# Performance work log

Hardware: AMD Instinct MI355X
Metric: run time of the kernel (lower is better)

The kernel has to match this reference:

```python
import jax, jax.numpy as jnp
import numpy as np
import math

HID = 256      # hidden_dim
POS = 32       # pos_dim (hardcoded num_pos_feats=32 in pos2embed call)
HEADS = 4
DH = HID // HEADS
B = 8          # number of ragged batches
N = 2048       # points per batch (inputs and queries, equal counts)
LN_EPS = 1e-5


def pos2embed(pos, num_pos_feats=POS):
    # pos: [..., 3] -> [..., 3*num_pos_feats]; faithfully keeps the original
    # bug where pos_z's cos half uses pos_x.
    pos = pos * (2.0 * math.pi)
    dim_t = jnp.arange(num_pos_feats, dtype=jnp.float32)
    dim_t = 2.0 * jnp.floor(dim_t / 2.0) / num_pos_feats + 1.0
    px = pos[..., 0, None] / dim_t
    py = pos[..., 1, None] / dim_t
    pz = pos[..., 2, None] / dim_t
    def interleave(s, c):
        return jnp.stack((s, c), axis=-1).reshape(*s.shape[:-1], -1)
    ex = interleave(jnp.sin(px[..., 0::2]), jnp.cos(px[..., 1::2]))
    ey = interleave(jnp.sin(py[..., 0::2]), jnp.cos(py[..., 1::2]))
    ez = interleave(jnp.sin(pz[..., 0::2]), jnp.cos(px[..., 1::2]))  # original bug
    return jnp.concatenate((ey, ex, ez), axis=-1)


def setup_inputs() -> dict:
    key = jax.random.key(0)
    ks = jax.random.split(key, 16)
    inputs = jax.random.normal(ks[0], (B * N, HID), jnp.float32)
    Q_in = jax.random.normal(ks[1], (B * N, HID), jnp.float32)
    bid = jnp.repeat(jnp.arange(B, dtype=jnp.float32), N)[:, None]
    input_coords = jnp.concatenate([bid, jax.random.uniform(ks[2], (B * N, 3), jnp.float32)], -1)
    Q_in_coords = jnp.concatenate([bid, jax.random.uniform(ks[3], (B * N, 3), jnp.float32)], -1)
    s = 0.02
    Wq = jax.random.normal(ks[4], (HID, HID + POS), jnp.float32) * s
    Wk = jax.random.normal(ks[5], (HID, HID + POS), jnp.float32) * s
    Wv = jax.random.normal(ks[6], (HID, HID + POS), jnp.float32) * s
    in_proj_w = jax.random.normal(ks[7], (3 * HID, HID), jnp.float32) * s
    in_proj_b = jnp.zeros((3 * HID,), jnp.float32)
    out_proj_w = jax.random.normal(ks[8], (HID, HID), jnp.float32) * s
    out_proj_b = jnp.zeros((HID,), jnp.float32)
    ln_g = jnp.ones((HID,), jnp.float32)
    ln_b = jnp.zeros((HID,), jnp.float32)
    pe_w1 = jax.random.normal(ks[9], (POS, POS * 3), jnp.float32) * s
    pe_b1 = jnp.zeros((POS,), jnp.float32)
    pe_w2 = jax.random.normal(ks[10], (POS, POS), jnp.float32) * s
    pe_b2 = jnp.zeros((POS,), jnp.float32)
    return dict(inputs=inputs, Q_in=Q_in, input_coords=input_coords, Q_in_coords=Q_in_coords,
                Wq=Wq, Wk=Wk, Wv=Wv, in_proj_w=in_proj_w, in_proj_b=in_proj_b,
                out_proj_w=out_proj_w, out_proj_b=out_proj_b, ln_g=ln_g, ln_b=ln_b,
                pe_w1=pe_w1, pe_b1=pe_b1, pe_w2=pe_w2, pe_b2=pe_b2)


def reference(inputs, Q_in, input_coords, Q_in_coords, Wq, Wk, Wv,
              in_proj_w, in_proj_b, out_proj_w, out_proj_b, ln_g, ln_b,
              pe_w1, pe_b1, pe_w2, pe_b2):
    # Equal per-batch counts let the ragged per-batch loop be one batched op.
    def pos_mlp(coords):  # [BN,4] -> [B,N,POS]
        e = pos2embed(coords[:, 1:], POS)                   # [BN, 3*POS]
        h = jax.nn.relu(e @ pe_w1.T + pe_b1)
        return (h @ pe_w2.T + pe_b2).reshape(B, N, POS)

    xb = inputs.reshape(B, N, HID)
    qb = Q_in.reshape(B, N, HID)
    ip = jnp.concatenate([xb, pos_mlp(input_coords)], -1)   # [B,N,HID+POS]
    qp = jnp.concatenate([qb, pos_mlp(Q_in_coords)], -1)

    Q = jnp.einsum('bnc,hc->bnh', qp, Wq)
    K = jnp.einsum('bnc,hc->bnh', ip, Wk)
    V = jnp.einsum('bnc,hc->bnh', ip, Wv)

    # nn.MultiheadAttention: its own in_proj on top of Q/K/V, then out_proj
    wq, wk, wv = in_proj_w[:HID], in_proj_w[HID:2 * HID], in_proj_w[2 * HID:]
    bq, bk, bv = in_proj_b[:HID], in_proj_b[HID:2 * HID], in_proj_b[2 * HID:]
    q = (Q @ wq.T + bq).reshape(B, N, HEADS, DH)
    k = (K @ wk.T + bk).reshape(B, N, HEADS, DH)
    v = (V @ wv.T + bv).reshape(B, N, HEADS, DH)

    scores = jnp.einsum('bqhd,bkhd->bhqk', q, k) / math.sqrt(DH)
    attn = jax.nn.softmax(scores, axis=-1)
    o = jnp.einsum('bhqk,bkhd->bqhd', attn, v).reshape(B, N, HID)
    o = o @ out_proj_w.T + out_proj_b

    # residual + LayerNorm (dropout is identity in eval)
    y = qb + o
    mu = y.mean(-1, keepdims=True)
    var = ((y - mu) ** 2).mean(-1, keepdims=True)
    yn = (y - mu) / jnp.sqrt(var + LN_EPS) * ln_g + ln_b
    return yn.reshape(B * N, HID)
```

## Files before the change

### kernel.cpp

```cpp
#include <hip/hip_runtime.h>
#include <math.h>

#define HID 256
#define CIN 288
#define NTOK 16384
#define NSEQ 2048
#define NH 4
#define DHD 64
#define TWO_PI 6.2831853071795864769f

typedef __attribute__((ext_vector_type(8))) short bf16x8;
typedef __attribute__((ext_vector_type(4))) float f32x4;
typedef __attribute__((ext_vector_type(4))) unsigned short u16x4;

__device__ __forceinline__ ushort f2bf(float x) {
    unsigned u = __float_as_uint(x);
    u = (u + 0x7FFFu + ((u >> 16) & 1u)) >> 16;
    return (ushort)u;
}

__device__ __forceinline__ float fast_exp2(float x) {
    return __builtin_amdgcn_exp2f(x);
}

__device__ __forceinline__ unsigned pack_bf_trunc(float a, float b) {
    return __builtin_amdgcn_perm(__float_as_uint(b), __float_as_uint(a), 0x07060302u);
}

__device__ __forceinline__ void gload_lds16(const ushort* g, ushort* l) {
    __builtin_amdgcn_global_load_lds(
        (const __attribute__((address_space(1))) unsigned*)g,
        (__attribute__((address_space(3))) unsigned*)l, 16, 0, 0);
}

__device__ __forceinline__ int sw(int row) {
    return (((row >> 3) << 1) ^ row) & 7;
}

__global__ void fuse_w_kernel(const float* __restrict__ inW,
                              const float* __restrict__ Wq,
                              const float* __restrict__ Wk,
                              const float* __restrict__ Wv,
                              ushort* __restrict__ Wb) {
    __shared__ float wrow[256];
    const int o = blockIdx.x;
    const int mat = blockIdx.y;
    const int t = threadIdx.x;
    if (t < 256) wrow[t] = inW[(mat * 256 + o) * 256 + t];
    __syncthreads();
    if (t >= CIN) return;
    const float* Wm = (mat == 0) ? Wq : ((mat == 1) ? Wk : Wv);
    float acc = 0.f;
#pragma unroll 4
    for (int h = 0; h < 256; ++h) acc += wrow[h] * Wm[h * CIN + t];
    Wb[(size_t)(mat * 256 + o) * CIN + t] = f2bf(acc);
}

__global__ void cast_wo(const float* __restrict__ Wo, ushort* __restrict__ WoB) {
    const int f = (blockIdx.x * 256 + threadIdx.x) * 4;
    const float4 a = *(const float4*)(Wo + f);
    u16x4 o = {f2bf(a.x), f2bf(a.y), f2bf(a.z), f2bf(a.w)};
    *(u16x4*)(WoB + f) = o;
}

__global__ __launch_bounds__(128) void pos_mlp_kernel(
        const float* __restrict__ icoords, const float* __restrict__ qcoords,
        const float* __restrict__ w1, const float* __restrict__ b1,
        const float* __restrict__ w2, const float* __restrict__ b2,
        ushort* __restrict__ ip, ushort* __restrict__ qp) {
    __shared__ float sw1t[96 * 32];
    __shared__ float sb1[32];
    __shared__ float sw2[32 * 32];
    __shared__ float sb2[32];
    const int t = threadIdx.x;
    for (int i = t; i < 96 * 32; i += 128) {
        const int e = i >> 5, r = i & 31;
        sw1t[i] = w1[r * 96 + e];
    }
    for (int i = t; i < 32 * 32; i += 128) sw2[i] = w2[i];
    if (t < 32) { sb1[t] = b1[t]; sb2[t] = b2[t]; }
    __syncthreads();

    const int tok = blockIdx.x * 128 + t;
    const int which = tok >> 14;
    const int m = tok & (NTOK - 1);
    const float* cr = (which ? qcoords : icoords) + m * 4;
    const float x = cr[1] * TWO_PI;
    const float y = cr[2] * TWO_PI;
    const float z = cr[3] * TWO_PI;

    f32x4 h4[8];
#pragma unroll
    for (int r4 = 0; r4 < 8; ++r4) h4[r4] = *(const f32x4*)&sb1[r4 * 4];

    for (int jj = 0; jj < 16; ++jj) {
        const float inv = 1.0f / (1.0f + 0.0625f * (float)jj);
        const float xs = x * inv, ys = y * inv, zs = z * inv;
        const float cx = __cosf(xs);
        float vals[6];
        int idx[6];
        vals[0] = __sinf(ys);  idx[0] = 2 * jj;
        vals[1] = __cosf(ys);  idx[1] = 2 * jj + 1;
        vals[2] = __sinf(xs);  idx[2] = 32 + 2 * jj;
        vals[3] = cx;          idx[3] = 32 + 2 * jj + 1;
        vals[4] = __sinf(zs);  idx[4] = 64 + 2 * jj;
        vals[5] = cx;          idx[5] = 64 + 2 * jj + 1;
#pragma unroll
        for (int u = 0; u < 6; ++u) {
            const float ev = vals[u];
            const f32x4* wr = (const f32x4*)&sw1t[idx[u] * 32];
#pragma unroll
            for (int r4 = 0; r4 < 8; ++r4) h4[r4] += ev * wr[r4];
        }
    }
#pragma unroll
    for (int r4 = 0; r4 < 8; ++r4)
#pragma unroll
        for (int j = 0; j < 4; ++j) h4[r4][j] = fmaxf(h4[r4][j], 0.f);

    ushort* dst = (which ? qp : ip) + (size_t)m * CIN + 256;
#pragma unroll
    for (int c = 0; c < 32; ++c) {
        const f32x4* w4 = (const f32x4*)&sw2[c * 32];
        f32x4 a4 = h4[0] * w4[0];
#pragma unroll
        for (int r4 = 1; r4 < 8; ++r4) a4 += h4[r4] * w4[r4];
        dst[c] = f2bf(sb2[c] + (a4[0] + a4[1]) + (a4[2] + a4[3]));
    }
}

__global__ void cast_x_kernel(const float* __restrict__ X, const float* __restrict__ Qin,
                              ushort* __restrict__ ip, ushort* __restrict__ qp) {
    const int which = blockIdx.y;
    const size_t f = ((size_t)blockIdx.x * 256 + threadIdx.x) * 8;
    const int row = (int)(f >> 8);
    const int col = (int)(f & 255);
    const float* src = which ? Qin : X;
    ushort* dst = which ? qp : ip;
    const float4 a = *(const float4*)(src + f);
    const float4 b = *(const float4*)(src + f + 4);
    u16x4 o0 = {f2bf(a.x), f2bf(a.y), f2bf(a.z), f2bf(a.w)};
    u16x4 o1 = {f2bf(b.x), f2bf(b.y), f2bf(b.z), f2bf(b.w)};
    *(u16x4*)(dst + (size_t)row * CIN + col) = o0;
    *(u16x4*)(dst + (size_t)row * CIN + col + 4) = o1;
}

__global__ __launch_bounds__(256) void qkv_mfma(
        const ushort* __restrict__ qp, const ushort* __restrict__ ip,
        const ushort* __restrict__ Wb, const float* __restrict__ bias,
        ushort* __restrict__ qout, ushort* __restrict__ kout, ushort* __restrict__ vout) {
    __shared__ ushort SA[2 * 4096];
    const int wv = threadIdx.x >> 6, lane = threadIdx.x & 63;
    const int l16 = lane & 15, quad = lane >> 4;
    const int m0b = blockIdx.x * 128;
    const int y = blockIdx.y;
    const int mat = y >> 2;
    const int n0 = y * 64;
    const ushort* A = (mat == 0) ? qp : ip;

    size_t asrc[2];
    int adst[2];
#pragma unroll
    for (int i = 0; i < 2; ++i) {
        const int idx = wv * 128 + i * 64 + lane;
        const int row = idx >> 2, cc = idx & 3;
        asrc[i] = (size_t)(m0b + row) * CIN + cc * 8;
        adst[i] = (wv * 128 + i * 64) * 8;
    }
    int aoff[2];
#pragma unroll
    for (int s = 0; s < 2; ++s)
        aoff[s] = ((32 * wv + 16 * s + l16) * 4 + quad) * 8;

    f32x4 acc[2][4];
#pragma unroll
    for (int s = 0; s < 2; ++s)
#pragma unroll
        for (int c = 0; c < 4; ++c) acc[s][c] = (f32x4){0.f, 0.f, 0.f, 0.f};

#pragma unroll
    for (int i = 0; i < 2; ++i)
        gload_lds16(A + asrc[i], SA + adst[i]);

    for (int t = 0; t < 9; ++t) {
        __syncthreads();
        if (t + 1 < 9) {
            const int bo = ((t + 1) & 1) * 4096;
#pragma unroll
            for (int i = 0; i < 2; ++i)
                gload_lds16(A + asrc[i] + (t + 1) * 32, SA + bo + adst[i]);
        }
        const ushort* buf = SA + (t & 1) * 4096;
        const int kk = t * 32;
        bf16x8 af[2], bf[4];
#pragma unroll
        for (int s = 0; s < 2; ++s)
            af[s] = *(const bf16x8*)(buf + aoff[s]);
#pragma unroll
        for (int c = 0; c < 4; ++c)
            bf[c] = *(const bf16x8*)(Wb + (size_t)(n0 + 16 * c + l16) * CIN + kk + quad * 8);
        if (mat < 2) {
#pragma unroll
            for (int s = 0; s < 2; ++s)
#pragma unroll
                for (int c = 0; c < 4; ++c)
                    acc[s][c] = __builtin_amdgcn_mfma_f32_16x16x32_bf16(bf[c], af[s], acc[s][c], 0, 0, 0);
        } else {
#pragma unroll
            for (int s = 0; s < 2; ++s)
#pragma unroll
                for (int c = 0; c < 4; ++c)
                    acc[s][c] = __builtin_amdgcn_mfma_f32_16x16x32_bf16(af[s], bf[c], acc[s][c], 0, 0, 0);
        }
    }

    const int h = y & 3;
    const int m0 = m0b + wv * 32;
    if (mat < 2) {
        const float scale = (mat == 0) ? (0.125f * 1.44269504088896f) : 1.0f;
        ushort* out = (mat == 0) ? qout : kout;
#pragma unroll
        for (int s = 0; s < 2; ++s) {
            const int tokm = m0 + 16 * s + l16;
            const int b = tokm >> 11, nn = tokm & (NSEQ - 1);
#pragma unroll
            for (int c = 0; c < 4; ++c) {
                const f32x4 b4 = *(const f32x4*)&bias[n0 + 16 * c + quad * 4];
                u16x4 w;
#pragma unroll
                for (int r = 0; r < 4; ++r) w[r] = f2bf((acc[s][c][r] + b4[r]) * scale);
                *(u16x4*)(out + ((size_t)(b * NH + h) * NSEQ + nn) * DHD + 16 * c + quad * 4) = w;
            }
        }
    } else {
#pragma unroll
        for (int s = 0; s < 2; ++s) {
            const int tok0 = m0 + 16 * s + quad * 4;
            const int b = tok0 >> 11, nn0 = tok0 & (NSEQ - 1);
#pragma unroll
            for (int c = 0; c < 4; ++c) {
                const int d = 16 * c + l16;
                const float bv = bias[n0 + d];
                u16x4 w;
#pragma unroll
                for (int r = 0; r < 4; ++r) w[r] = f2bf(acc[s][c][r] + bv);
                *(u16x4*)(vout + ((size_t)(b * NH + h) * DHD + d) * NSEQ + nn0) = w;
            }
        }
    }
}

__global__ __launch_bounds__(256) void attn_kernel(
        const ushort* __restrict__ q, const ushort* __restrict__ k,
        const ushort* __restrict__ v, ushort* __restrict__ out) {
    __shared__ ushort SL[2 * 8192];
    const int bh = blockIdx.y;
    const int wv = threadIdx.x >> 6;
    const int lane = threadIdx.x & 63;
    const int l16 = lane & 15, quad = lane >> 4;
    const int q0 = blockIdx.x * 128 + wv * 32;

    const ushort* qb = q + (size_t)bh * NSEQ * DHD;
    const ushort* kb = k + (size_t)bh * NSEQ * DHD;
    const ushort* vb = v + (size_t)bh * DHD * NSEQ;

    bf16x8 qf[2][2];
#pragma unroll
    for (int s = 0; s < 2; ++s)
#pragma unroll
        for (int hh = 0; hh < 2; ++hh)
            qf[s][hh] = *(const bf16x8*)(qb + (size_t)(q0 + 16 * s + l16) * DHD + 32 * hh + quad * 8);

    int ksrc[2], vsrc[2], sdst[2];
#pragma unroll
    for (int i = 0; i < 2; ++i) {
        const int idx = wv * 128 + i * 64 + lane;
        const int row = idx >> 3;
        const int cg = (idx & 7) ^ sw(row);
        ksrc[i] = row * DHD + cg * 8;
        vsrc[i] = row * NSEQ + cg * 8;
        sdst[i] = (wv * 128 + i * 64) * 8;
    }

    const int krow = 8 * (l16 >> 2) + (l16 & 3);
    int koff[2][2][2];
    int voff[2][4];
#pragma unroll
    for (int sub = 0; sub < 2; ++sub) {
#pragma unroll
        for (int m = 0; m < 2; ++m) {
            const int row = sub * 32 + krow + 4 * m;
#pragma unroll
            for (int hh = 0; hh < 2; ++hh)
                koff[sub][m][hh] = (row * 8 + ((hh * 4 + quad) ^ sw(row))) * 8;
        }
#pragma unroll
        for (int c = 0; c < 4; ++c) {
            const int row = 16 * c + l16;
            voff[sub][c] = 4096 + (row * 8 + ((sub * 4 + quad) ^ sw(row))) * 8;
        }
    }

    f32x4 Oc[2][4];
#pragma unroll
    for (int s = 0; s < 2; ++s)
#pragma unroll
        for (int c = 0; c < 4; ++c) Oc[s][c] = (f32x4){0.f, 0.f, 0.f, 0.f};
    float lrun[2] = {0.f, 0.f};

#pragma unroll
    for (int i = 0; i < 2; ++i) {
        gload_lds16(kb + ksrc[i], SL + sdst[i]);
        gload_lds16(vb + vsrc[i], SL + 4096 + sdst[i]);
    }

    for (int t = 0; t < 32; ++t) {
        __syncthreads();
        if (t + 1 < 32) {
            const int bo = ((t + 1) & 1) * 8192;
            const int kt = (t + 1) * 64;
#pragma unroll
            for (int i = 0; i < 2; ++i) {
                gload_lds16(kb + (size_t)kt * DHD + ksrc[i], SL + bo + sdst[i]);
                gload_lds16(vb + kt + vsrc[i], SL + bo + 4096 + sdst[i]);
            }
        }
        const ushort* buf = SL + (t & 1) * 8192;

#pragma unroll
        for (int sub = 0; sub < 2; ++sub) {
            bf16x8 kf[2][2], vf[4];
#pragma unroll
            for (int m = 0; m < 2; ++m)
#pragma unroll
                for (int hh = 0; hh < 2; ++hh)
                    kf[m][hh] = *(const bf16x8*)(buf + koff[sub][m][hh]);
#pragma unroll
            for (int c = 0; c < 4; ++c)
                vf[c] = *(const bf16x8*)(buf + voff[sub][c]);

#pragma unroll
            for (int s = 0; s < 2; ++s) {
                f32x4 s0 = (f32x4){0.f, 0.f, 0.f, 0.f};
                f32x4 s1 = (f32x4){0.f, 0.f, 0.f, 0.f};
                s0 = __builtin_amdgcn_mfma_f32_16x16x32_bf16(kf[0][0], qf[s][0], s0, 0, 0, 0);
                s0 = __builtin_amdgcn_mfma_f32_16x16x32_bf16(kf[0][1], qf[s][1], s0, 0, 0, 0);
                s1 = __builtin_amdgcn_mfma_f32_16x16x32_bf16(kf[1][0], qf[s][0], s1, 0, 0, 0);
                s1 = __builtin_amdgcn_mfma_f32_16x16x32_bf16(kf[1][1], qf[s][1], s1, 0, 0, 0);

                float p0[4], p1[4];
#pragma unroll
                for (int r = 0; r < 4; ++r) {
                    p0[r] = fast_exp2(s0[r]);
                    p1[r] = fast_exp2(s1[r]);
                }
                lrun[s] += (p0[0] + p0[1]) + (p0[2] + p0[3]) + (p1[0] + p1[1]) + (p1[2] + p1[3]);

                union { bf16x8 v8; unsigned d[4]; } P;
                P.d[0] = pack_bf_trunc(p0[0], p0[1]);
                P.d[1] = pack_bf_trunc(p0[2], p0[3]);
                P.d[2] = pack_bf_trunc(p1[0], p1[1]);
                P.d[3] = pack_bf_trunc(p1[2], p1[3]);
#pragma unroll
                for (int c = 0; c < 4; ++c)
                    Oc[s][c] = __builtin_amdgcn_mfma_f32_16x16x32_bf16(vf[c], P.v8, Oc[s][c], 0, 0, 0);
            }
        }
    }

    const int b = bh >> 2, h = bh & 3;
#pragma unroll
    for (int s = 0; s < 2; ++s) {
        float ls = lrun[s];
        ls += __shfl_xor(ls, 16);
        ls += __shfl_xor(ls, 32);
        const float linv = 1.0f / ls;
        ushort* dst = out + (size_t)(b * NSEQ + q0 + 16 * s + l16) * HID + h * DHD;
#pragma unroll
        for (int c = 0; c < 4; ++c) {
            u16x4 w;
#pragma unroll
            for (int r = 0; r < 4; ++r) w[r] = f2bf(Oc[s][c][r] * linv);
            *(u16x4*)(dst + 16 * c + quad * 4) = w;
        }
    }
}

__global__ __launch_bounds__(256) void oproj_ln_mfma(
        const ushort* __restrict__ abuf, const float* __restrict__ Qin,
        const ushort* __restrict__ WoB, const float* __restrict__ bo,
        const float* __restrict__ g, const float* __restrict__ be,
        float* __restrict__ out) {
    __shared__ float yt[32][260];
    const int wv = threadIdx.x >> 6, lane = threadIdx.x & 63;
    const int l16 = lane & 15, quad = lane >> 4;
    const int m0 = blockIdx.x * 32;
    const int n0 = wv * 64;

    f32x4 acc[2][4];
#pragma unroll
    for (int s = 0; s < 2; ++s)
#pragma unroll
        for (int c = 0; c < 4; ++c) acc[s][c] = (f32x4){0.f, 0.f, 0.f, 0.f};

    for (int kk = 0; kk < HID; kk += 32) {
        bf16x8 af[2], bf[4];
#pragma unroll
        for (int s = 0; s < 2; ++s)
            af[s] = *(const bf16x8*)(abuf + (size_t)(m0 + 16 * s + l16) * HID + kk + quad * 8);
#pragma unroll
        for (int c = 0; c < 4; ++c)
            bf[c] = *(const bf16x8*)(WoB + (size_t)(n0 + 16 * c + l16) * HID + kk + quad * 8);
#pragma unroll
        for (int s = 0; s < 2; ++s)
#pragma unroll
            for (int c = 0; c < 4; ++c)
                acc[s][c] = __builtin_amdgcn_mfma_f32_16x16x32_bf16(af[s], bf[c], acc[s][c], 0, 0, 0);
    }

#pragma unroll
    for (int s = 0; s < 2; ++s)
#pragma unroll
        for (int c = 0; c < 4; ++c) {
            const int col = n0 + 16 * c + l16;
            const float bv = bo[col];
#pragma unroll
            for (int r = 0; r < 4; ++r) {
                const int row = 16 * s + quad * 4 + r;
                yt[row][col] = acc[s][c][r] + bv + Qin[(size_t)(m0 + row) * HID + col];
            }
        }
    __syncthreads();

    float gv[4], bev[4];
#pragma unroll
    for (int u = 0; u < 4; ++u) { gv[u] = g[lane + 64 * u]; bev[u] = be[lane + 64 * u]; }

    for (int rr = 0; rr < 8; ++rr) {
        const int row = wv * 8 + rr;
        float sm = 0.f, ssq = 0.f;
        float yv[4];
#pragma unroll
        for (int u = 0; u < 4; ++u) {
            yv[u] = yt[row][lane + 64 * u];
            sm += yv[u]; ssq += yv[u] * yv[u];
        }
#pragma unroll
        for (int off = 32; off >= 1; off >>= 1) {
            sm += __shfl_xor(sm, off);
            ssq += __shfl_xor(ssq, off);
        }
        const float mu = sm * (1.f / 256.f);
        const float rs = rsqrtf(fmaxf(ssq * (1.f / 256.f) - mu * mu, 0.f) + 1e-5f);
        float* dst = out + (size_t)(m0 + row) * HID;
#pragma unroll
        for (int u = 0; u < 4; ++u)
            dst[lane + 64 * u] = (yv[u] - mu) * rs * gv[u] + bev[u];
    }
}

extern "C" void kernel_launch(void* const* d_in, const int* in_sizes, int n_in,
                              void* d_out, int out_size, void* d_ws, size_t ws_size,
                              hipStream_t stream) {
    const float* inputs       = (const float*)d_in[0];
    const float* Q_in         = (const float*)d_in[1];
    const float* input_coords = (const float*)d_in[2];
    const float* Q_in_coords  = (const float*)d_in[3];
    const float* Wq           = (const float*)d_in[4];
    const float* Wk           = (const float*)d_in[5];
    const float* Wv           = (const float*)d_in[6];
    const float* in_proj_w    = (const float*)d_in[7];
    const float* in_proj_b    = (const float*)d_in[8];
    const float* out_proj_w   = (const float*)d_in[9];
    const float* out_proj_b   = (const float*)d_in[10];
    const float* ln_g         = (const float*)d_in[11];
    const float* ln_b         = (const float*)d_in[12];
    const float* pe_w1        = (const float*)d_in[13];
    const float* pe_b1        = (const float*)d_in[14];
    const float* pe_w2        = (const float*)d_in[15];
    const float* pe_b2        = (const float*)d_in[16];

    char* ws = (char*)d_ws;
    ushort* Wb   = (ushort*)(ws);
    ushort* WoB  = (ushort*)(ws + 442368);
    ushort* qp   = (ushort*)(ws + 573440);
    ushort* ip   = (ushort*)(ws + 10010624);
    ushort* qbuf = (ushort*)(ws + 19447808);
    ushort* kbuf = (ushort*)(ws + 27836416);
    ushort* vbuf = (ushort*)(ws + 36225024);
    ushort* abuf = (ushort*)(ws + 44613632);

    fuse_w_kernel<<<dim3(256, 3), 320, 0, stream>>>(in_proj_w, Wq, Wk, Wv, Wb);
    cast_wo<<<64, 256, 0, stream>>>(out_proj_w, WoB);
    pos_mlp_kernel<<<256, 128, 0, stream>>>(input_coords, Q_in_coords,
                                            pe_w1, pe_b1, pe_w2, pe_b2, ip, qp);
    cast_x_kernel<<<dim3(2048, 2), 256, 0, stream>>>(inputs, Q_in, ip, qp);
    qkv_mfma<<<dim3(128, 12), 256, 0, stream>>>(qp, ip, Wb, in_proj_b,
                                                qbuf, kbuf, vbuf);
    attn_kernel<<<dim3(16, 32), 256, 0, stream>>>(qbuf, kbuf, vbuf, abuf);
    oproj_ln_mfma<<<512, 256, 0, stream>>>(abuf, Q_in, WoB, out_proj_b,
                                           ln_g, ln_b, (float*)d_out);
}
```

Baseline: 232.7 us.

## Split attention over two KV halves and merge partials in out-projection

The attention kernel now launches a third grid dimension, and each block handles half of the key/value sequence. This doubles the block count from 512 to 1024 so more of the GPU is occupied. Unnormalized fp32 partial outputs and row sums are written per half, and the out-projection kernel adds them, normalizes and casts to bf16 before its MFMA. The row sum is now computed with an MFMA against a ones vector instead of scalar adds. In exchange, fp32 partials roughly quadruple the intermediate traffic compared with the bf16 attention output. The merge is valid without a running-max rescale only because the softmax uses no max subtraction, as in the earlier code.

Measured after the change: 251.2 us. +8.0%, slower.

```diff
diff --git a/kernel.cpp b/kernel.cpp
--- a/kernel.cpp
+++ b/kernel.cpp
@@ -252,9 +252,12 @@
 
 __global__ __launch_bounds__(256) void attn_kernel(
         const ushort* __restrict__ q, const ushort* __restrict__ k,
-        const ushort* __restrict__ v, ushort* __restrict__ out) {
+        const ushort* __restrict__ v,
+        float* __restrict__ O0p, float* __restrict__ O1p,
+        float* __restrict__ ls0, float* __restrict__ ls1) {
     __shared__ ushort SL[2 * 8192];
     const int bh = blockIdx.y;
+    const int half = blockIdx.z;
     const int wv = threadIdx.x >> 6;
     const int lane = threadIdx.x & 63;
     const int l16 = lane & 15, quad = lane >> 4;
@@ -306,19 +309,25 @@
     for (int s = 0; s < 2; ++s)
 #pragma unroll
         for (int c = 0; c < 4; ++c) Oc[s][c] = (f32x4){0.f, 0.f, 0.f, 0.f};
-    float lrun[2] = {0.f, 0.f};
+    f32x4 Lc[2];
+#pragma unroll
+    for (int s = 0; s < 2; ++s) Lc[s] = (f32x4){0.f, 0.f, 0.f, 0.f};
+    const short ob = (short)0x3F80;
+    const bf16x8 onesf = {ob, ob, ob, ob, ob, ob, ob, ob};
+
+    const int kbase = half * (NSEQ / 2);
 
 #pragma unroll
     for (int i = 0; i < 2; ++i) {
-        gload_lds16(kb + ksrc[i], SL + sdst[i]);
-        gload_lds16(vb + vsrc[i], SL + 4096 + sdst[i]);
-    }
-
-    for (int t = 0; t < 32; ++t) {
+        gload_lds16(kb + (size_t)kbase * DHD + ksrc[i], SL + sdst[i]);
+        gload_lds16(vb + kbase + vsrc[i], SL + 4096 + sdst[i]);
+    }
+
+    for (int t = 0; t < 16; ++t) {
         __syncthreads();
-        if (t + 1 < 32) {
+        if (t + 1 < 16) {
             const int bo = ((t + 1) & 1) * 8192;
-            const int kt = (t + 1) * 64;
+            const int kt = kbase + (t + 1) * 64;
 #pragma unroll
             for (int i = 0; i < 2; ++i) {
                 gload_lds16(kb + (size_t)kt * DHD + ksrc[i], SL + bo + sdst[i]);
@@ -354,13 +363,13 @@
                     p0[r] = fast_exp2(s0[r]);
                     p1[r] = fast_exp2(s1[r]);
                 }
-                lrun[s] += (p0[0] + p0[1]) + (p0[2] + p0[3]) + (p1[0] + p1[1]) + (p1[2] + p1[3]);
 
                 union { bf16x8 v8; unsigned d[4]; } P;
                 P.d[0] = pack_bf_trunc(p0[0], p0[1]);
                 P.d[1] = pack_bf_trunc(p0[2], p0[3]);
                 P.d[2] = pack_bf_trunc(p1[0], p1[1]);
                 P.d[3] = pack_bf_trunc(p1[2], p1[3]);
+                Lc[s] = __builtin_amdgcn_mfma_f32_16x16x32_bf16(onesf, P.v8, Lc[s], 0, 0, 0);
 #pragma unroll
                 for (int c = 0; c < 4; ++c)
                     Oc[s][c] = __builtin_amdgcn_mfma_f32_16x16x32_bf16(vf[c], P.v8, Oc[s][c], 0, 0, 0);
@@ -369,25 +378,23 @@
     }
 
     const int b = bh >> 2, h = bh & 3;
+    float* Op = half ? O1p : O0p;
+    float* lsum = half ? ls1 : ls0;
 #pragma unroll
     for (int s = 0; s < 2; ++s) {
-        float ls = lrun[s];
-        ls += __shfl_xor(ls, 16);
-        ls += __shfl_xor(ls, 32);
-        const float linv = 1.0f / ls;
-        ushort* dst = out + (size_t)(b * NSEQ + q0 + 16 * s + l16) * HID + h * DHD;
-#pragma unroll
-        for (int c = 0; c < 4; ++c) {
-            u16x4 w;
-#pragma unroll
-            for (int r = 0; r < 4; ++r) w[r] = f2bf(Oc[s][c][r] * linv);
-            *(u16x4*)(dst + 16 * c + quad * 4) = w;
-        }
+        const int query = q0 + 16 * s + l16;
+        if (quad == 0) lsum[bh * NSEQ + query] = Lc[s][0];
+        float* dst = Op + (size_t)(b * NSEQ + query) * HID + h * DHD;
+#pragma unroll
+        for (int c = 0; c < 4; ++c)
+            *(f32x4*)(dst + 16 * c + quad * 4) = Oc[s][c];
     }
 }
 
 __global__ __launch_bounds__(256) void oproj_ln_mfma(
-        const ushort* __restrict__ abuf, const float* __restrict__ Qin,
+        const float* __restrict__ O0p, const float* __restrict__ O1p,
+        const float* __restrict__ ls0, const float* __restrict__ ls1,
+        const float* __restrict__ Qin,
         const ushort* __restrict__ WoB, const float* __restrict__ bo,
         const float* __restrict__ g, const float* __restrict__ be,
         float* __restrict__ out) {
@@ -397,6 +404,18 @@
     const int m0 = blockIdx.x * 32;
     const int n0 = wv * 64;
 
+    float linv[2][4];
+#pragma unroll
+    for (int s = 0; s < 2; ++s) {
+        const int tok = m0 + 16 * s + l16;
+        const int b = tok >> 11, nn = tok & (NSEQ - 1);
+#pragma unroll
+        for (int h = 0; h < 4; ++h) {
+            const int idx = (b * NH + h) * NSEQ + nn;
+            linv[s][h] = 1.0f / (ls0[idx] + ls1[idx]);
+        }
+    }
+
     f32x4 acc[2][4];
 #pragma unroll
     for (int s = 0; s < 2; ++s)
@@ -404,10 +423,23 @@
         for (int c = 0; c < 4; ++c) acc[s][c] = (f32x4){0.f, 0.f, 0.f, 0.f};
 
     for (int kk = 0; kk < HID; kk += 32) {
+        const int hd = kk >> 6;
         bf16x8 af[2], bf[4];
 #pragma unroll
-        for (int s = 0; s < 2; ++s)
-            af[s] = *(const bf16x8*)(abuf + (size_t)(m0 + 16 * s + l16) * HID + kk + quad * 8);
+        for (int s = 0; s < 2; ++s) {
+            const size_t base = (size_t)(m0 + 16 * s + l16) * HID + kk + quad * 8;
+            const f32x4 x0 = *(const f32x4*)(O0p + base);
+            const f32x4 x1 = *(const f32x4*)(O0p + base + 4);
+            const f32x4 y0 = *(const f32x4*)(O1p + base);
+            const f32x4 y1 = *(const f32x4*)(O1p + base + 4);
+            const float li = linv[s][hd];
+            union { bf16x8 v8; u16x4 hx[2]; } A;
+#pragma unroll
+            for (int j = 0; j < 4; ++j) A.hx[0][j] = f2bf((x0[j] + y0[j]) * li);
+#pragma unroll
+            for (int j = 0; j < 4; ++j) A.hx[1][j] = f2bf((x1[j] + y1[j]) * li);
+            af[s] = A.v8;
+        }
 #pragma unroll
         for (int c = 0; c < 4; ++c)
             bf[c] = *(const bf16x8*)(WoB + (size_t)(n0 + 16 * c + l16) * HID + kk + quad * 8);
@@ -488,7 +520,10 @@
     ushort* qbuf = (ushort*)(ws + 19447808);
     ushort* kbuf = (ushort*)(ws + 27836416);
     ushort* vbuf = (ushort*)(ws + 36225024);
-    ushort* abuf = (ushort*)(ws + 44613632);
+    float* O0    = (float*)(ws + 573440);
+    float* O1    = (float*)(ws + 44613632);
+    float* ls0   = (float*)(ws + 61390848);
+    float* ls1   = (float*)(ws + 61456384);
 
     fuse_w_kernel<<<dim3(256, 3), 320, 0, stream>>>(in_proj_w, Wq, Wk, Wv, Wb);
     cast_wo<<<64, 256, 0, stream>>>(out_proj_w, WoB);
@@ -497,7 +532,8 @@
     cast_x_kernel<<<dim3(2048, 2), 256, 0, stream>>>(inputs, Q_in, ip, qp);
     qkv_mfma<<<dim3(128, 12), 256, 0, stream>>>(qp, ip, Wb, in_proj_b,
                                                 qbuf, kbuf, vbuf);
-    attn_kernel<<<dim3(16, 32), 256, 0, stream>>>(qbuf, kbuf, vbuf, abuf);
-    oproj_ln_mfma<<<512, 256, 0, stream>>>(abuf, Q_in, WoB, out_proj_b,
-                                           ln_g, ln_b, (float*)d_out);
-}
+    attn_kernel<<<dim3(16, 32, 2), 256, 0, stream>>>(qbuf, kbuf, vbuf,
+                                                     O0, O1, ls0, ls1);
+    oproj_ln_mfma<<<512, 256, 0, stream>>>(O0, O1, ls0, ls1, Q_in, WoB,
+                                           out_proj_b, ln_g, ln_b, (float*)d_out);
+}
```

## Deepen attention K/V LDS pipeline to four buffers and sum softmax with MFMA

Applied to the files above, without the earlier changes.

The attention kernel moves from double-buffered K/V tiles in LDS to a four-slot ring that prefetches three tiles ahead. It replaces __syncthreads with explicit vmcnt waits plus s_barrier, and unrolls the loop by four so buffer indices are compile-time constants. The softmax row sum is now built by an extra MFMA against a ones vector, which removes the per-lane adds and the final shuffle reduction. LDS use doubles to 64KB per block, which may lower occupancy, and the row sum now comes from bf16-truncated probabilities.

New measurement: 233.1 us. Within noise of the previous version (+0.2%).

```diff
diff --git a/kernel.cpp b/kernel.cpp
--- a/kernel.cpp
+++ b/kernel.cpp
@@ -253,7 +253,7 @@
 __global__ __launch_bounds__(256) void attn_kernel(
         const ushort* __restrict__ q, const ushort* __restrict__ k,
         const ushort* __restrict__ v, ushort* __restrict__ out) {
-    __shared__ ushort SL[2 * 8192];
+    __shared__ ushort SL[4 * 8192];
     const int bh = blockIdx.y;
     const int wv = threadIdx.x >> 6;
     const int lane = threadIdx.x & 63;
@@ -306,64 +306,82 @@
     for (int s = 0; s < 2; ++s)
 #pragma unroll
         for (int c = 0; c < 4; ++c) Oc[s][c] = (f32x4){0.f, 0.f, 0.f, 0.f};
-    float lrun[2] = {0.f, 0.f};
-
-#pragma unroll
-    for (int i = 0; i < 2; ++i) {
-        gload_lds16(kb + ksrc[i], SL + sdst[i]);
-        gload_lds16(vb + vsrc[i], SL + 4096 + sdst[i]);
-    }
-
-    for (int t = 0; t < 32; ++t) {
-        __syncthreads();
-        if (t + 1 < 32) {
-            const int bo = ((t + 1) & 1) * 8192;
-            const int kt = (t + 1) * 64;
-#pragma unroll
-            for (int i = 0; i < 2; ++i) {
-                gload_lds16(kb + (size_t)kt * DHD + ksrc[i], SL + bo + sdst[i]);
-                gload_lds16(vb + kt + vsrc[i], SL + bo + 4096 + sdst[i]);
+    f32x4 Lc[2];
+#pragma unroll
+    for (int s = 0; s < 2; ++s) Lc[s] = (f32x4){0.f, 0.f, 0.f, 0.f};
+    const short ob = (short)0x3F80;
+    const bf16x8 onesf = {ob, ob, ob, ob, ob, ob, ob, ob};
+
+#pragma unroll
+    for (int pt = 0; pt < 3; ++pt) {
+        ushort* db = SL + pt * 8192;
+#pragma unroll
+        for (int i = 0; i < 2; ++i) {
+            gload_lds16(kb + (size_t)pt * (64 * DHD) + ksrc[i], db + sdst[i]);
+            gload_lds16(vb + pt * 64 + vsrc[i], db + 4096 + sdst[i]);
+        }
+    }
+
+    for (int tb = 0; tb < 32; tb += 4) {
+#pragma unroll
+        for (int u = 0; u < 4; ++u) {
+            const int t = tb + u;
+            if (t < 30)       asm volatile("s_waitcnt vmcnt(8)" ::: "memory");
+            else if (t == 30) asm volatile("s_waitcnt vmcnt(4)" ::: "memory");
+            else              asm volatile("s_waitcnt vmcnt(0)" ::: "memory");
+            __builtin_amdgcn_s_barrier();
+
+            if (t < 29) {
+                const int pf = t + 3;
+                ushort* db = SL + ((u + 3) & 3) * 8192;
+                const ushort* kpt = kb + (size_t)pf * (64 * DHD);
+                const ushort* vpt = vb + pf * 64;
+#pragma unroll
+                for (int i = 0; i < 2; ++i) {
+                    gload_lds16(kpt + ksrc[i], db + sdst[i]);
+                    gload_lds16(vpt + vsrc[i], db + 4096 + sdst[i]);
+                }
             }
-        }
-        const ushort* buf = SL + (t & 1) * 8192;
-
-#pragma unroll
-        for (int sub = 0; sub < 2; ++sub) {
-            bf16x8 kf[2][2], vf[4];
-#pragma unroll
-            for (int m = 0; m < 2; ++m)
-#pragma unroll
-                for (int hh = 0; hh < 2; ++hh)
-                    kf[m][hh] = *(const bf16x8*)(buf + koff[sub][m][hh]);
-#pragma unroll
-            for (int c = 0; c < 4; ++c)
-                vf[c] = *(const bf16x8*)(buf + voff[sub][c]);
-
-#pragma unroll
-            for (int s = 0; s < 2; ++s) {
-                f32x4 s0 = (f32x4){0.f, 0.f, 0.f, 0.f};
-                f32x4 s1 = (f32x4){0.f, 0.f, 0.f, 0.f};
-                s0 = __builtin_amdgcn_mfma_f32_16x16x32_bf16(kf[0][0], qf[s][0], s0, 0, 0, 0);
-                s0 = __builtin_amdgcn_mfma_f32_16x16x32_bf16(kf[0][1], qf[s][1], s0, 0, 0, 0);
-                s1 = __builtin_amdgcn_mfma_f32_16x16x32_bf16(kf[1][0], qf[s][0], s1, 0, 0, 0);
-                s1 = __builtin_amdgcn_mfma_f32_16x16x32_bf16(kf[1][1], qf[s][1], s1, 0, 0, 0);
-
-                float p0[4], p1[4];
-#pragma unroll
-                for (int r = 0; r < 4; ++r) {
-                    p0[r] = fast_exp2(s0[r]);
-                    p1[r] = fast_exp2(s1[r]);
+            const ushort* buf = SL + u * 8192;
+
+#pragma unroll
+            for (int sub = 0; sub < 2; ++sub) {
+                bf16x8 kf[2][2], vf[4];
+#pragma unroll
+                for (int m = 0; m < 2; ++m)
+#pragma unroll
+                    for (int hh = 0; hh < 2; ++hh)
+                        kf[m][hh] = *(const bf16x8*)(buf + koff[sub][m][hh]);
+#pragma unroll
+                for (int c = 0; c < 4; ++c)
+                    vf[c] = *(const bf16x8*)(buf + voff[sub][c]);
+
+#pragma unroll
+                for (int s = 0; s < 2; ++s) {
+                    f32x4 s0 = (f32x4){0.f, 0.f, 0.f, 0.f};
+                    f32x4 s1 = (f32x4){0.f, 0.f, 0.f, 0.f};
+                    s0 = __builtin_amdgcn_mfma_f32_16x16x32_bf16(kf[0][0], qf[s][0], s0, 0, 0, 0);
+                    s0 = __builtin_amdgcn_mfma_f32_16x16x32_bf16(kf[0][1], qf[s][1], s0, 0, 0, 0);
+                    s1 = __builtin_amdgcn_mfma_f32_16x16x32_bf16(kf[1][0], qf[s][0], s1, 0, 0, 0);
+                    s1 = __builtin_amdgcn_mfma_f32_16x16x32_bf16(kf[1][1], qf[s][1], s1, 0, 0, 0);
+
+                    float p0[4], p1[4];
+#pragma unroll
+                    for (int r = 0; r < 4; ++r) {
+                        p0[r] = fast_exp2(s0[r]);
+                        p1[r] = fast_exp2(s1[r]);
+                    }
+
+                    union { bf16x8 v8; unsigned d[4]; } P;
+                    P.d[0] = pack_bf_trunc(p0[0], p0[1]);
+                    P.d[1] = pack_bf_trunc(p0[2], p0[3]);
+                    P.d[2] = pack_bf_trunc(p1[0], p1[1]);
+                    P.d[3] = pack_bf_trunc(p1[2], p1[3]);
+                    Lc[s] = __builtin_amdgcn_mfma_f32_16x16x32_bf16(onesf, P.v8, Lc[s], 0, 0, 0);
+#pragma unroll
+                    for (int c = 0; c < 4; ++c)
+                        Oc[s][c] = __builtin_amdgcn_mfma_f32_16x16x32_bf16(vf[c], P.v8, Oc[s][c], 0, 0, 0);
                 }
-                lrun[s] += (p0[0] + p0[1]) + (p0[2] + p0[3]) + (p1[0] + p1[1]) + (p1[2] + p1[3]);
-
-                union { bf16x8 v8; unsigned d[4]; } P;
-                P.d[0] = pack_bf_trunc(p0[0], p0[1]);
-                P.d[1] = pack_bf_trunc(p0[2], p0[3]);
-                P.d[2] = pack_bf_trunc(p1[0], p1[1]);
-                P.d[3] = pack_bf_trunc(p1[2], p1[3]);
-#pragma unroll
-                for (int c = 0; c < 4; ++c)
-                    Oc[s][c] = __builtin_amdgcn_mfma_f32_16x16x32_bf16(vf[c], P.v8, Oc[s][c], 0, 0, 0);
             }
         }
     }
@@ -371,10 +389,7 @@
     const int b = bh >> 2, h = bh & 3;
 #pragma unroll
     for (int s = 0; s < 2; ++s) {
-        float ls = lrun[s];
-        ls += __shfl_xor(ls, 16);
-        ls += __shfl_xor(ls, 32);
-        const float linv = 1.0f / ls;
+        const float linv = 1.0f / Lc[s][0];
         ushort* dst = out + (size_t)(b * NSEQ + q0 + 16 * s + l16) * HID + h * DHD;
 #pragma unroll
         for (int c = 0; c < 4; ++c) {
```

## Split attention KV range across two wave groups with triple-buffered LDS

Applied to the files above, without the earlier changes.

The attention block grows to 512 threads, and two groups of four waves each process half of the key sequence for the same 128 queries. Their partial outputs and row sums are combined through LDS at the end. Each group uses a 3-stage ring of 32-key tiles loaded with global_load_lds, synchronized with explicit vmcnt waits and raw barriers, and the V tile uses a new swizzle. The goal is more waves in flight per CU to hide latency, at the cost of an extra LDS reduction step and smaller tiles per barrier.

After: 230.5 us. No clear change (-0.9%).

```diff
diff --git a/kernel.cpp b/kernel.cpp
--- a/kernel.cpp
+++ b/kernel.cpp
@@ -35,6 +35,10 @@
 
 __device__ __forceinline__ int sw(int row) {
     return (((row >> 3) << 1) ^ row) & 7;
+}
+
+__device__ __forceinline__ int swv(int row) {
+    return ((row & 3) ^ ((row >> 2) & 3));
 }
 
 __global__ void fuse_w_kernel(const float* __restrict__ inW,
@@ -250,19 +254,22 @@
     }
 }
 
-__global__ __launch_bounds__(256) void attn_kernel(
+__global__ __launch_bounds__(512, 4) void attn_kernel(
         const ushort* __restrict__ q, const ushort* __restrict__ k,
         const ushort* __restrict__ v, ushort* __restrict__ out) {
-    __shared__ ushort SL[2 * 8192];
+    __shared__ ushort SL[24576];
     const int bh = blockIdx.y;
     const int wv = threadIdx.x >> 6;
+    const int grp = wv >> 2;
+    const int wq = wv & 3;
     const int lane = threadIdx.x & 63;
     const int l16 = lane & 15, quad = lane >> 4;
-    const int q0 = blockIdx.x * 128 + wv * 32;
+    const int q0 = blockIdx.x * 128 + wq * 32;
 
     const ushort* qb = q + (size_t)bh * NSEQ * DHD;
-    const ushort* kb = k + (size_t)bh * NSEQ * DHD;
-    const ushort* vb = v + (size_t)bh * DHD * NSEQ;
+    const ushort* kb = k + (size_t)bh * NSEQ * DHD + (size_t)(grp * 1024) * DHD;
+    const ushort* vb = v + (size_t)bh * DHD * NSEQ + grp * 1024;
+    ushort* SG = SL + grp * 12288;
 
     bf16x8 qf[2][2];
 #pragma unroll
@@ -271,117 +278,133 @@
         for (int hh = 0; hh < 2; ++hh)
             qf[s][hh] = *(const bf16x8*)(qb + (size_t)(q0 + 16 * s + l16) * DHD + 32 * hh + quad * 8);
 
-    int ksrc[2], vsrc[2], sdst[2];
-#pragma unroll
-    for (int i = 0; i < 2; ++i) {
-        const int idx = wv * 128 + i * 64 + lane;
-        const int row = idx >> 3;
-        const int cg = (idx & 7) ^ sw(row);
-        ksrc[i] = row * DHD + cg * 8;
-        vsrc[i] = row * NSEQ + cg * 8;
-        sdst[i] = (wv * 128 + i * 64) * 8;
-    }
+    const int krow_s = 8 * wq + (lane >> 3);
+    const int kcg = (lane & 7) ^ sw(krow_s);
+    const size_t ksrc = (size_t)krow_s * DHD + kcg * 8;
+    const int kdst = wq * 512;
+    const int vrow_s = 16 * wq + (lane >> 2);
+    const int vcg = (lane & 3) ^ swv(vrow_s);
+    const size_t vsrc = (size_t)vrow_s * NSEQ + vcg * 8;
+    const int vdst = wq * 512;
 
     const int krow = 8 * (l16 >> 2) + (l16 & 3);
-    int koff[2][2][2];
-    int voff[2][4];
-#pragma unroll
-    for (int sub = 0; sub < 2; ++sub) {
-#pragma unroll
-        for (int m = 0; m < 2; ++m) {
-            const int row = sub * 32 + krow + 4 * m;
+    int koff[2][2];
+    int voff[4];
+#pragma unroll
+    for (int m = 0; m < 2; ++m) {
+        const int row = krow + 4 * m;
+#pragma unroll
+        for (int hh = 0; hh < 2; ++hh)
+            koff[m][hh] = row * 64 + (((hh * 4 + quad) ^ sw(row))) * 8;
+    }
+#pragma unroll
+    for (int c = 0; c < 4; ++c) {
+        const int d = 16 * c + l16;
+        voff[c] = 2048 + d * 32 + ((quad ^ swv(d))) * 8;
+    }
+
+    f32x4 Oc[2][4];
+#pragma unroll
+    for (int s = 0; s < 2; ++s)
+#pragma unroll
+        for (int c = 0; c < 4; ++c) Oc[s][c] = (f32x4){0.f, 0.f, 0.f, 0.f};
+    float lr[2] = {0.f, 0.f};
+
+#pragma unroll
+    for (int pt = 0; pt < 2; ++pt) {
+        ushort* db = SG + pt * 4096;
+        gload_lds16(kb + (size_t)(pt * 32) * DHD + ksrc, db + kdst);
+        gload_lds16(vb + pt * 32 + vsrc, db + 2048 + vdst);
+    }
+
+    int co = 0, po = 8192;
+    for (int t = 0; t < 32; ++t) {
+        if (t < 31) asm volatile("s_waitcnt vmcnt(2)" ::: "memory");
+        else        asm volatile("s_waitcnt vmcnt(0)" ::: "memory");
+        __builtin_amdgcn_s_barrier();
+
+        if (t < 30) {
+            ushort* db = SG + po;
+            gload_lds16(kb + (size_t)((t + 2) * 32) * DHD + ksrc, db + kdst);
+            gload_lds16(vb + (t + 2) * 32 + vsrc, db + 2048 + vdst);
+            po = (po == 8192) ? 0 : po + 4096;
+        }
+        const ushort* buf = SG + co;
+        co = (co == 8192) ? 0 : co + 4096;
+
+        bf16x8 kf[2][2], vf[4];
+#pragma unroll
+        for (int m = 0; m < 2; ++m)
 #pragma unroll
             for (int hh = 0; hh < 2; ++hh)
-                koff[sub][m][hh] = (row * 8 + ((hh * 4 + quad) ^ sw(row))) * 8;
-        }
-#pragma unroll
-        for (int c = 0; c < 4; ++c) {
-            const int row = 16 * c + l16;
-            voff[sub][c] = 4096 + (row * 8 + ((sub * 4 + quad) ^ sw(row))) * 8;
-        }
-    }
-
-    f32x4 Oc[2][4];
-#pragma unroll
-    for (int s = 0; s < 2; ++s)
-#pragma unroll
-        for (int c = 0; c < 4; ++c) Oc[s][c] = (f32x4){0.f, 0.f, 0.f, 0.f};
-    float lrun[2] = {0.f, 0.f};
-
-#pragma unroll
-    for (int i = 0; i < 2; ++i) {
-        gload_lds16(kb + ksrc[i], SL + sdst[i]);
-        gload_lds16(vb + vsrc[i], SL + 4096 + sdst[i]);
-    }
-
-    for (int t = 0; t < 32; ++t) {
-        __syncthreads();
-        if (t + 1 < 32) {
-            const int bo = ((t + 1) & 1) * 8192;
-            const int kt = (t + 1) * 64;
-#pragma unroll
-            for (int i = 0; i < 2; ++i) {
-                gload_lds16(kb + (size_t)kt * DHD + ksrc[i], SL + bo + sdst[i]);
-                gload_lds16(vb + kt + vsrc[i], SL + bo + 4096 + sdst[i]);
+                kf[m][hh] = *(const bf16x8*)(buf + koff[m][hh]);
+#pragma unroll
+        for (int c = 0; c < 4; ++c)
+            vf[c] = *(const bf16x8*)(buf + voff[c]);
+
+#pragma unroll
+        for (int s = 0; s < 2; ++s) {
+            f32x4 s0 = (f32x4){0.f, 0.f, 0.f, 0.f};
+            f32x4 s1 = (f32x4){0.f, 0.f, 0.f, 0.f};
+            s0 = __builtin_amdgcn_mfma_f32_16x16x32_bf16(kf[0][0], qf[s][0], s0, 0, 0, 0);
+            s0 = __builtin_amdgcn_mfma_f32_16x16x32_bf16(kf[0][1], qf[s][1], s0, 0, 0, 0);
+            s1 = __builtin_amdgcn_mfma_f32_16x16x32_bf16(kf[1][0], qf[s][0], s1, 0, 0, 0);
+            s1 = __builtin_amdgcn_mfma_f32_16x16x32_bf16(kf[1][1], qf[s][1], s1, 0, 0, 0);
+
+            float p0[4], p1[4];
+#pragma unroll
+            for (int r = 0; r < 4; ++r) {
+                p0[r] = fast_exp2(s0[r]);
+                p1[r] = fast_exp2(s1[r]);
             }
-        }
-        const ushort* buf = SL + (t & 1) * 8192;
-
-#pragma unroll
-        for (int sub = 0; sub < 2; ++sub) {
-            bf16x8 kf[2][2], vf[4];
-#pragma unroll
-            for (int m = 0; m < 2; ++m)
-#pragma unroll
-                for (int hh = 0; hh < 2; ++hh)
-                    kf[m][hh] = *(const bf16x8*)(buf + koff[sub][m][hh]);
+            lr[s] += (p0[0] + p0[1]) + (p0[2] + p0[3]) + (p1[0] + p1[1]) + (p1[2] + p1[3]);
+
+            union { bf16x8 v8; unsigned d[4]; } P;
+            P.d[0] = pack_bf_trunc(p0[0], p0[1]);
+            P.d[1] = pack_bf_trunc(p0[2], p0[3]);
+            P.d[2] = pack_bf_trunc(p1[0], p1[1]);
+            P.d[3] = pack_bf_trunc(p1[2], p1[3]);
 #pragma unroll
             for (int c = 0; c < 4; ++c)
-                vf[c] = *(const bf16x8*)(buf + voff[sub][c]);
-
-#pragma unroll
-            for (int s = 0; s < 2; ++s) {
-                f32x4 s0 = (f32x4){0.f, 0.f, 0.f, 0.f};
-                f32x4 s1 = (f32x4){0.f, 0.f, 0.f, 0.f};
-                s0 = __builtin_amdgcn_mfma_f32_16x16x32_bf16(kf[0][0], qf[s][0], s0, 0, 0, 0);
-                s0 = __builtin_amdgcn_mfma_f32_16x16x32_bf16(kf[0][1], qf[s][1], s0, 0, 0, 0);
-                s1 = __builtin_amdgcn_mfma_f32_16x16x32_bf16(kf[1][0], qf[s][0], s1, 0, 0, 0);
-                s1 = __builtin_amdgcn_mfma_f32_16x16x32_bf16(kf[1][1], qf[s][1], s1, 0, 0, 0);
-
-                float p0[4], p1[4];
-#pragma unroll
-                for (int r = 0; r < 4; ++r) {
-                    p0[r] = fast_exp2(s0[r]);
-                    p1[r] = fast_exp2(s1[r]);
-                }
-                lrun[s] += (p0[0] + p0[1]) + (p0[2] + p0[3]) + (p1[0] + p1[1]) + (p1[2] + p1[3]);
-
-                union { bf16x8 v8; unsigned d[4]; } P;
-                P.d[0] = pack_bf_trunc(p0[0], p0[1]);
-                P.d[1] = pack_bf_trunc(p0[2], p0[3]);
-                P.d[2] = pack_bf_trunc(p1[0], p1[1]);
-                P.d[3] = pack_bf_trunc(p1[2], p1[3]);
-#pragma unroll
-                for (int c = 0; c < 4; ++c)
-                    Oc[s][c] = __builtin_amdgcn_mfma_f32_16x16x32_bf16(vf[c], P.v8, Oc[s][c], 0, 0, 0);
+                Oc[s][c] = __builtin_amdgcn_mfma_f32_16x16x32_bf16(vf[c], P.v8, Oc[s][c], 0, 0, 0);
+        }
+    }
+
+#pragma unroll
+    for (int s = 0; s < 2; ++s) {
+        lr[s] += __shfl_xor(lr[s], 16);
+        lr[s] += __shfl_xor(lr[s], 32);
+    }
+
+    __syncthreads();
+    float* exch = (float*)SL;
+    float* lx   = ((float*)SL) + 128 * 68;
+    if (grp == 1) {
+#pragma unroll
+        for (int s = 0; s < 2; ++s) {
+            const int lq = wq * 32 + 16 * s + l16;
+#pragma unroll
+            for (int c = 0; c < 4; ++c)
+                *(f32x4*)&exch[lq * 68 + 16 * c + 4 * quad] = Oc[s][c];
+            if (quad == 0) lx[lq] = lr[s];
+        }
+    }
+    __syncthreads();
+    if (grp == 0) {
+        const int b = bh >> 2, h = bh & 3;
+#pragma unroll
+        for (int s = 0; s < 2; ++s) {
+            const int lq = wq * 32 + 16 * s + l16;
+            const float linv = 1.0f / (lr[s] + lx[lq]);
+            ushort* dst = out + (size_t)(b * NSEQ + blockIdx.x * 128 + lq) * HID + h * DHD;
+#pragma unroll
+            for (int c = 0; c < 4; ++c) {
+                const f32x4 o1 = *(const f32x4*)&exch[lq * 68 + 16 * c + 4 * quad];
+                u16x4 w;
+#pragma unroll
+                for (int r = 0; r < 4; ++r) w[r] = f2bf((Oc[s][c][r] + o1[r]) * linv);
+                *(u16x4*)(dst + 16 * c + quad * 4) = w;
             }
-        }
-    }
-
-    const int b = bh >> 2, h = bh & 3;
-#pragma unroll
-    for (int s = 0; s < 2; ++s) {
-        float ls = lrun[s];
-        ls += __shfl_xor(ls, 16);
-        ls += __shfl_xor(ls, 32);
-        const float linv = 1.0f / ls;
-        ushort* dst = out + (size_t)(b * NSEQ + q0 + 16 * s + l16) * HID + h * DHD;
-#pragma unroll
-        for (int c = 0; c < 4; ++c) {
-            u16x4 w;
-#pragma unroll
-            for (int r = 0; r < 4; ++r) w[r] = f2bf(Oc[s][c][r] * linv);
-            *(u16x4*)(dst + 16 * c + quad * 4) = w;
         }
     }
 }
@@ -497,7 +520,7 @@
     cast_x_kernel<<<dim3(2048, 2), 256, 0, stream>>>(inputs, Q_in, ip, qp);
     qkv_mfma<<<dim3(128, 12), 256, 0, stream>>>(qp, ip, Wb, in_proj_b,
                                                 qbuf, kbuf, vbuf);
-    attn_kernel<<<dim3(16, 32), 256, 0, stream>>>(qbuf, kbuf, vbuf, abuf);
+    attn_kernel<<<dim3(16, 32), 512, 0, stream>>>(qbuf, kbuf, vbuf, abuf);
     oproj_ln_mfma<<<512, 256, 0, stream>>>(abuf, Q_in, WoB, out_proj_b,
                                            ln_g, ln_b, (float*)d_out);
 }
```
